# Kernel tuning notes

Measured on AMD Instinct MI355X. Metric: run time of the kernel, lower is better.

The kernel has to match this reference:

```python
import math
import jax, jax.numpy as jnp
import numpy as np

# ---- static config (mirrors init_kwargs) ----
NLAT_I, NLON_I = 240, 480      # input equiangular grid (incl. both poles)
NLAT_O, NLON_O = 361, 720      # output equiangular grid (incl. both poles)
CI, CO = 32, 32
NR, NPHI = 3, 3                # kernel_shape
K = (NR - 1) * NPHI + 1        # anisotropic piecewise-linear DISCO basis size = 7
LMAX = 120
CUTOFF = (NR + 0.25) * math.pi / LMAX     # _compute_cutoff_radius
DLAT_O = math.pi / (NLAT_O - 1)
WOFF = int(math.ceil(CUTOFF / DLAT_O))    # half lat-window (=10); geodesic dist >= |dtheta| so window is exact
WLAT = 2 * WOFF + 1
TWO_PI = 2.0 * math.pi


def _bilinear_upsample(x):
    # ResampleS2(mode='bilinear'): x [B,C,NLAT_I,NLON_I] -> [B,C,NLAT_O,NLON_O]
    # equiangular colatitudes theta_j = pi*j/(nlat-1); periodic longitude.
    pos_t = jnp.linspace(0.0, math.pi, NLAT_O) / (math.pi / (NLAT_I - 1))
    i0 = jnp.clip(jnp.floor(pos_t).astype(jnp.int32), 0, NLAT_I - 1)
    i1 = jnp.minimum(i0 + 1, NLAT_I - 1)
    wt = (pos_t - i0).astype(x.dtype)
    xl = (1.0 - wt)[:, None] * x[:, :, i0, :] + wt[:, None] * x[:, :, i1, :]
    pos_p = (jnp.arange(NLON_O) * (TWO_PI / NLON_O)) / (TWO_PI / NLON_I)
    j0f = jnp.floor(pos_p)
    j0 = j0f.astype(jnp.int32) % NLON_I
    j1 = (j0 + 1) % NLON_I
    wp = (pos_p - j0f).astype(x.dtype)
    return (1.0 - wp) * xl[..., j0] + wp * xl[..., j1]


def _build_psi():
    # DISCO filter tensor psi[k, t_out, dlat, dlon] with quadrature merged in,
    # exploiting longitude translation invariance (computed at lon_out = 0).
    theta = jnp.linspace(0.0, math.pi, NLAT_O)
    t_idx = jnp.arange(NLAT_O)
    d_idx = jnp.arange(WLAT) - WOFF
    lat_in = t_idx[:, None] + d_idx[None, :]             # [T,W]
    valid = (lat_in >= 0) & (lat_in < NLAT_O)
    lat_in_c = jnp.clip(lat_in, 0, NLAT_O - 1)
    alpha = -theta[:, None, None]                         # [T,1,1]
    gamma = theta[lat_in_c][:, :, None]                   # [T,W,1]
    beta = (TWO_PI / NLON_O) * jnp.arange(NLON_O)[None, None, :]
    # rotate input point into frame where the output point is at the north pole
    z = jnp.cos(alpha) * jnp.cos(gamma) - jnp.cos(beta) * jnp.sin(alpha) * jnp.sin(gamma)
    xx = jnp.cos(alpha) * jnp.cos(beta) * jnp.sin(gamma) + jnp.sin(alpha) * jnp.cos(gamma)
    yy = jnp.sin(beta) * jnp.sin(gamma)
    r = jnp.arccos(jnp.clip(z, -1.0, 1.0))                # geodesic distance [T,W,P]
    phi = jnp.arctan2(yy, xx) % TWO_PI                    # local azimuth
    dr = CUTOFF / NR
    dph = TWO_PI / NPHI
    vals = [jnp.maximum(0.0, 1.0 - r / dr)]               # isotropic center hat
    for k in range(1, K):
        ir = (k - 1) // NPHI + 1
        ip = (k - 1) % NPHI
        rad = jnp.maximum(0.0, 1.0 - jnp.abs(r - ir * dr) / dr)
        dd = jnp.abs(phi - ip * dph)
        dd = jnp.minimum(dd, TWO_PI - dd)
        az = jnp.maximum(0.0, 1.0 - dd / dph)
        vals.append(rad * az)
    psi = jnp.stack(vals, 0)                              # [K,T,W,P]
    psi = psi * (r <= CUTOFF) * valid[None, :, :, None]
    # merge quadrature weights of the input grid (sin(theta) dtheta dphi)
    q = jnp.sin(theta) * (math.pi / (NLAT_O - 1)) * (TWO_PI / NLON_O)
    psi = psi * q[lat_in_c][None, :, :, None]
    # nodal L1 normalization per basis function and output node
    scale = jnp.sum(psi, axis=(2, 3), keepdims=True)
    psi = psi / jnp.maximum(scale, 1e-8)
    return psi.astype(jnp.float32), lat_in_c


def _disco_conv(xu, weight, psi, lat_in_c):
    # xu [B,Ci,T,P]; weight [Co,Ci,K]; psi [K,T,W,P]
    h = jnp.einsum('oik,bitp->boktp', weight, xu)         # fold channel mixing first
    Hh = jnp.fft.rfft(h, axis=-1)                         # [B,Co,K,T,F]
    Ph = jnp.conj(jnp.fft.rfft(psi, axis=-1))             # [K,T,W,F]
    yh = jnp.zeros(Hh.shape[:2] + (NLAT_O, Hh.shape[-1]), dtype=Hh.dtype)
    for d in range(WLAT):                                 # small fixed halo loop
        Hd = Hh[:, :, :, lat_in_c[:, d], :]               # [B,Co,K,T,F]
        yh = yh + jnp.einsum('boktf,ktf->botf', Hd, Ph[:, :, d, :])
    return jnp.fft.irfft(yh, n=NLON_O, axis=-1)           # circular correlation over lon


def setup_inputs() -> dict:
    key = jax.random.key(0)
    k1, k2 = jax.random.split(key)
    x = jax.random.normal(k1, (1, CI, NLAT_I, NLON_I), dtype=jnp.float32)
    weight = jax.random.normal(k2, (CO, CI, K), dtype=jnp.float32) * 0.05
    return {'x': x, 'weight': weight}


def reference(x, weight):
    psi, lat_in_c = _build_psi()
    xu = _bilinear_upsample(x.astype(jnp.float32))        # forced fp32 region
    y = _disco_conv(xu, weight.astype(jnp.float32), psi, lat_in_c)
    return y.astype(x.dtype)
```

## Files before the change

kernel.cpp:

```cpp
#include <hip/hip_runtime.h>
#include <hip/hip_bf16.h>
#include <math.h>

#define NLAT_I 240
#define NLON_I 480
#define NLAT_O 361
#define NLON_O 720
#define CI_N 32
#define CO_N 32
#define K_N 7
#define WOFF 10
#define WLAT 21

#define PI_F 3.14159265358979323846f
#define TWOPI_F 6.28318530717958647692f
#define DLAT_V (PI_F / 360.0f)
#define DPHI_V (TWOPI_F / 720.0f)
#define CUTOFF_V (3.25f * PI_F / 120.0f)
#define DR_V (CUTOFF_V / 3.0f)
#define IDR_V (1.0f / DR_V)
#define DPH_V (TWOPI_F / 3.0f)
#define IDPH_V (1.0f / DPH_V)
#define QF_V (DLAT_V * DPHI_V)

#define PAD_T 64
#define CT 64
#define NBLK 512
#define NC45 45
#define NE 7581

typedef __attribute__((ext_vector_type(8))) short short8v;
typedef __attribute__((ext_vector_type(16))) float f32x16;

__device__ __forceinline__ unsigned short f2bf(float f) {
  __hip_bfloat16 h = __float2bfloat16(f);
  union { __hip_bfloat16 b; unsigned short s; } u; u.b = h; return u.s;
}

__device__ __forceinline__ void psi_eval(float ct, float st, float cg, float sg,
                                         float q, float bang, float v[7]) {
  float sb, cb;
  sincosf(bang, &sb, &cb);
  float dx = sg * cb - st;
  float dy = sg * sb;
  float dz = cg - ct;
  float c2 = dx * dx + dy * dy + dz * dz;
  float r = 2.0f * asinf(fminf(1.0f, 0.5f * sqrtf(c2)));
  if (r <= CUTOFF_V) {
    float xx = ct * cb * sg - st * cg;
    float yy = sb * sg;
    float phi = atan2f(yy, xx);
    if (phi < 0.0f) phi += TWOPI_F;
    v[0] = fmaxf(0.0f, 1.0f - r * IDR_V) * q;
#pragma unroll
    for (int k = 1; k < 7; ++k) {
      const float irdr = (float)(1 + (k - 1) / 3) * DR_V;
      const float ipph = (float)((k - 1) % 3) * DPH_V;
      float rad = fmaxf(0.0f, 1.0f - fabsf(r - irdr) * IDR_V);
      float dd = fabsf(phi - ipph);
      dd = fminf(dd, TWOPI_F - dd);
      float az = fmaxf(0.0f, 1.0f - dd * IDPH_V);
      v[k] = rad * az * q;
    }
  } else {
#pragma unroll
    for (int k = 0; k < 7; ++k) v[k] = 0.0f;
  }
}

__device__ __forceinline__ int windowB(int t, int d) {
  int tp = t + d - WOFF;
  if (tp < 0 || tp > NLAT_O - 1) return -1;
  float th = (float)t * DLAT_V, ga = (float)tp * DLAT_V;
  float st = sinf(th), ct = cosf(th), sg = sinf(ga), cg = cosf(ga);
  float den = st * sg;
  float num = cosf(CUTOFF_V) - ct * cg;
  if (den < 1e-9f) return (fabsf(th - ga) <= CUTOFF_V) ? 360 : -1;
  if (num >= den) return -1;
  if (num <= -den) return 360;
  int B = (int)ceilf(acosf(num / den) * (1.0f / DPHI_V)) + 1;
  return B > 360 ? 360 : B;
}

__device__ __forceinline__ int nsupOf(int B) { return (B >= 360) ? 720 : 2 * B + 1; }
__device__ __forceinline__ int widthOf(int B) {
  return (B < 0) ? 0 : ((nsupOf(B) + 129) & ~1);
}

__global__ void prep_kernel(const float* __restrict__ w, unsigned short* __restrict__ w2,
                            int* __restrict__ offsF, int* __restrict__ offsT,
                            int* __restrict__ wtab, float* __restrict__ sums,
                            int* __restrict__ counter) {
  const int tid = threadIdx.x;
  __shared__ int temp[256];
  if (tid == 0) *counter = 0;
  for (int idx = tid; idx < 361 * 7; idx += 256) sums[idx] = 0.0f;
  for (int idx = tid; idx < 14 * 32 * 16; idx += 256) {
    int kk = idx & 15; int o = (idx >> 4) & 31; int c16 = idx >> 9;
    int ci = c16 * 16 + kk; int i = ci & 31; int k = ci >> 5;
    w2[idx] = f2bf(w[(o * 32 + i) * 7 + k]);
  }
  for (int e = tid; e < NE; e += 256) {
    int t = e / 21, d = e % 21;
    int B = windowB(t, d);
    offsF[e] = (B >= 0) ? nsupOf(B) * 7 : 0;
    offsT[e] = 14 * widthOf(B);
  }
  for (int t = tid; t < 361; t += 256) {
    int Wt = 0;
    for (int d = 0; d < WLAT; ++d) {
      int B = windowB(t, d);
      if (B >= 0) Wt += ((31 + B) >> 4) + ((B + 15) >> 4) + 1;
    }
    wtab[t] = Wt;
  }
  __syncthreads();
#pragma unroll 1
  for (int pass = 0; pass < 2; ++pass) {
    int* a = pass ? offsT : offsF;
    int s = tid * 30, e = s + 30; if (e > NE) e = NE; if (s > NE) s = NE;
    int sum = 0;
    for (int i = s; i < e; ++i) sum += a[i];
    temp[tid] = sum;
    __syncthreads();
    if (tid == 0) {
      int run = 0;
      for (int i = 0; i < 256; ++i) { int v = temp[i]; temp[i] = run; run += v; }
      a[NE] = run;
    }
    __syncthreads();
    int run = temp[tid];
    for (int i = s; i < e; ++i) { int v = a[i]; a[i] = run; run += v; }
    __syncthreads();
  }
}

__global__ void upsample_kernel(const float* __restrict__ x,
                                unsigned short* __restrict__ XT) {
  int idx = blockIdx.x * 256 + threadIdx.x;
  if (idx >= NLAT_O * NC45 * 512) return;
  int kk = idx & 15;
  int i = (idx >> 4) & 31;
  int c = (idx >> 9) % NC45;
  int t = idx / (NC45 * 512);
  int p = c * 16 + kk;

  double post = (double)t * (239.0 / 360.0);
  int i0 = (int)floor(post);
  if (i0 < 0) i0 = 0;
  if (i0 > NLAT_I - 1) i0 = NLAT_I - 1;
  int i1 = i0 + 1; if (i1 > NLAT_I - 1) i1 = NLAT_I - 1;
  float wt = (float)(post - (double)i0);

  double posp = (double)p * (2.0 / 3.0);
  double j0f = floor(posp);
  int j0 = ((int)j0f) % NLON_I;
  int j1 = (j0 + 1) % NLON_I;
  float wp = (float)(posp - j0f);

  const float* xi = x + (size_t)i * (NLAT_I * NLON_I);
  float a = xi[i0 * NLON_I + j0];
  float b = xi[i0 * NLON_I + j1];
  float cc = xi[i1 * NLON_I + j0];
  float d = xi[i1 * NLON_I + j1];
  float l0 = (1.0f - wt) * a + wt * cc;
  float l1 = (1.0f - wt) * b + wt * d;
  XT[idx] = f2bf((1.0f - wp) * l0 + wp * l1);
}

__global__ void psi_raw_kernel(const int* __restrict__ offsF,
                               float* __restrict__ PSIF,
                               float* __restrict__ sums) {
  int t = blockIdx.x, d = blockIdx.y;
  int B = windowB(t, d);
  if (B < 0) return;
  int nsup = nsupOf(B);
  int bLo = (B >= 360) ? -360 : -B;
  int offF = offsF[t * 21 + d];
  int tp = t + d - WOFF;
  float th = (float)t * DLAT_V, ga = (float)tp * DLAT_V;
  float st, ct, sg, cg;
  sincosf(th, &st, &ct);
  sincosf(ga, &sg, &cg);
  float q = sg * QF_V;
  float acc[7];
#pragma unroll
  for (int k = 0; k < 7; ++k) acc[k] = 0.0f;
  for (int ix = threadIdx.x; ix < nsup; ix += 256) {
    float v[7];
    psi_eval(ct, st, cg, sg, q, (float)(bLo + ix) * DPHI_V, v);
#pragma unroll
    for (int k = 0; k < 7; ++k) { PSIF[offF + k * nsup + ix] = v[k]; acc[k] += v[k]; }
  }
#pragma unroll
  for (int k = 0; k < 7; ++k) {
    float a = acc[k];
    for (int off = 32; off > 0; off >>= 1) a += __shfl_down(a, off, 64);
    acc[k] = a;
  }
  __shared__ float red[4][7];
  int wid = threadIdx.x >> 6;
  if ((threadIdx.x & 63) == 0) {
#pragma unroll
    for (int k = 0; k < 7; ++k) red[wid][k] = acc[k];
  }
  __syncthreads();
  if (threadIdx.x == 0) {
#pragma unroll
    for (int k = 0; k < 7; ++k)
      atomicAdd(&sums[t * 7 + k], red[0][k] + red[1][k] + red[2][k] + red[3][k]);
  }
}

__global__ void psi_toep_kernel(const int* __restrict__ offsF,
                                const int* __restrict__ offsT,
                                const float* __restrict__ PSIF,
                                const float* __restrict__ sums,
                                unsigned short* __restrict__ PSIT) {
  int t = blockIdx.x, d = blockIdx.y;
  int B = windowB(t, d);
  if (B < 0) return;
  int nsup = nsupOf(B);
  int width = widthOf(B);
  int offF = offsF[t * 21 + d];
  int offT = offsT[t * 21 + d];
  float rc[7];
#pragma unroll
  for (int k = 0; k < 7; ++k) rc[k] = 1.0f / fmaxf(sums[t * 7 + k], 1e-8f);
  for (int ix = threadIdx.x; ix <= width; ix += 256) {
    int isup = ix - PAD_T;
    unsigned short vv[7];
    if (isup >= 0 && isup < nsup) {
#pragma unroll
      for (int k = 0; k < 7; ++k)
        vv[k] = f2bf(PSIF[offF + k * nsup + isup] * rc[k]);
    } else {
#pragma unroll
      for (int k = 0; k < 7; ++k) vv[k] = 0;
    }
    if (ix < width) {
#pragma unroll
      for (int k = 0; k < 7; ++k) PSIT[offT + (2 * k) * width + ix] = vv[k];
    }
    if (ix >= 1) {
#pragma unroll
      for (int k = 0; k < 7; ++k) PSIT[offT + (2 * k + 1) * width + ix - 1] = vv[k];
    }
  }
}

#define LOADSET(S, CC) {                                                  \
    int v45 = pw16 + (CC);                                                \
    if (v45 < 0) v45 += NC45;                                             \
    if (v45 >= NC45) v45 -= NC45;                                         \
    A##S = *(const short8v*)(XT + (((size_t)tpd * NC45 + v45) << 9) + laneA); \
    int jbIdx = (CC) * 16 + lconst - bLo + PAD_T;                         \
    const unsigned short* bp = pbase + jbIdx + ((jbIdx & 1) ? (wdt - 1) : 0); \
    B##S##0 = *(const short8v*)(bp);                                      \
    B##S##1 = *(const short8v*)(bp + ks);                                 \
    B##S##2 = *(const short8v*)(bp + 2 * ks);                             \
    B##S##3 = *(const short8v*)(bp + 3 * ks);                             \
    B##S##4 = *(const short8v*)(bp + 4 * ks);                             \
    B##S##5 = *(const short8v*)(bp + 5 * ks);                             \
    B##S##6 = *(const short8v*)(bp + 6 * ks); }

#define MFMASET(S) {                                                      \
    acc0 = __builtin_amdgcn_mfma_f32_32x32x16_bf16(A##S, B##S##0, acc0, 0, 0, 0); \
    acc1 = __builtin_amdgcn_mfma_f32_32x32x16_bf16(A##S, B##S##1, acc1, 0, 0, 0); \
    acc2 = __builtin_amdgcn_mfma_f32_32x32x16_bf16(A##S, B##S##2, acc2, 0, 0, 0); \
    acc3 = __builtin_amdgcn_mfma_f32_32x32x16_bf16(A##S, B##S##3, acc3, 0, 0, 0); \
    acc4 = __builtin_amdgcn_mfma_f32_32x32x16_bf16(A##S, B##S##4, acc4, 0, 0, 0); \
    acc5 = __builtin_amdgcn_mfma_f32_32x32x16_bf16(A##S, B##S##5, acc5, 0, 0, 0); \
    acc6 = __builtin_amdgcn_mfma_f32_32x32x16_bf16(A##S, B##S##6, acc6, 0, 0, 0); }

#define DUMPQ(RR) {                                                       \
    int iq = ((RR) & 3) + 8 * ((RR) >> 2) + 4 * g;                        \
    int base = nn * 16 + (iq & 15);                                       \
    b2[0*512+base] = f2bf(acc0[RR]); b2[1*512+base] = f2bf(acc1[RR]);     \
    b2[2*512+base] = f2bf(acc2[RR]); b2[3*512+base] = f2bf(acc3[RR]);     \
    b2[4*512+base] = f2bf(acc4[RR]); b2[5*512+base] = f2bf(acc5[RR]);     \
    b2[6*512+base] = f2bf(acc6[RR]); }

__global__ __launch_bounds__(256, 2) void disco_kernel(
    const unsigned short* __restrict__ XT, const unsigned short* __restrict__ PSIT,
    const unsigned short* __restrict__ w2g, const int* __restrict__ offsT,
    const int* __restrict__ wtab, float* __restrict__ y,
    int* __restrict__ counter) {
  const int tid = threadIdx.x;
  __shared__ __align__(16) unsigned short b2all[4 * 3584];
  __shared__ int Sbuf[362];
  __shared__ int sB[WLAT], sUc[WLAT + 1], sOff[WLAT], sW[WLAT];
  __shared__ int curItem;

  for (int j = tid; j < 361; j += 256) {
    int t = (j & 1) ? 360 - (j >> 1) : (j >> 1);
    Sbuf[j] = 6 * ((wtab[t] + CT - 1) / CT);
  }
  __syncthreads();
  if (tid == 0) {
    int run = 0;
    for (int j = 0; j < 361; ++j) { int v = Sbuf[j]; Sbuf[j] = run; run += v; }
    Sbuf[361] = run;
  }
  __syncthreads();
  const int NTOT = Sbuf[361];

  const int lane = tid & 63, wv = tid >> 6, nn = lane & 31, g = lane >> 5;
  const int g8 = g * 8;
  const int laneA = nn * 16 + g8;
  const int lconst = g8 - nn;

  while (true) {
    if (tid == 0) curItem = atomicAdd(counter, 1);
    __syncthreads();
    const int m = curItem;
    if (m >= NTOT) break;

    int lo = 0, hi = 360;
    while (lo < hi) {
      int mid = (lo + hi + 1) >> 1;
      if (Sbuf[mid] <= m) lo = mid; else hi = mid - 1;
    }
    const int j = lo;
    const int r = m - Sbuf[j];
    const int t = (j & 1) ? 360 - (j >> 1) : (j >> 1);
    const int pgroup = r % 6;
    const int part = r / 6;

    if (tid < WLAT) {
      int B = windowB(t, tid);
      sB[tid] = B;
      sOff[tid] = offsT[t * 21 + tid];
      sW[tid] = widthOf(B);
    }
    __syncthreads();
    if (tid == 0) {
      int run = 0; sUc[0] = 0;
      for (int d = 0; d < WLAT; ++d) {
        int B = sB[d];
        int np = (B >= 0) ? ((31 + B) >> 4) + ((B + 15) >> 4) + 1 : 0;
        run += np; sUc[d + 1] = run;
      }
    }
    __syncthreads();
    const int Wt = sUc[WLAT];
    int g0 = part * CT, g1 = g0 + CT;
    if (g1 > Wt) g1 = Wt;

    const int ptile = pgroup * 4 + wv;
    const int pw = ptile * 32;
    const int pw16 = ptile * 2;

    f32x16 acc0, acc1, acc2, acc3, acc4, acc5, acc6;
#pragma unroll
    for (int z = 0; z < 16; ++z) {
      acc0[z]=0; acc1[z]=0; acc2[z]=0; acc3[z]=0; acc4[z]=0; acc5[z]=0; acc6[z]=0;
    }

    short8v A0, A1;
    short8v B00, B01, B02, B03, B04, B05, B06;
    short8v B10, B11, B12, B13, B14, B15, B16;

    int gi = g0;
    int d = 0;
    while (d < WLAT && sUc[d + 1] <= gi) ++d;
    while (gi < g1) {
      const int B = sB[d];
      const int bLo = (B >= 360) ? -360 : -B;
      const int cmin = -((B + 15) >> 4);
      const int tpd = t + d - WOFF;
      const int wdt = sW[d];
      const int ks = 2 * wdt;
      const unsigned short* pbase = PSIT + sOff[d];
      const int rend = sUc[d + 1];
      const int gend = (rend < g1) ? rend : g1;
      const int n = gend - gi;
      int c = cmin + (gi - sUc[d]);

      LOADSET(0, c)
      int it = 0;
      for (; it + 2 <= n; it += 2) {
        LOADSET(1, c + 1)
        MFMASET(0)
        if (it + 2 < n) { LOADSET(0, c + 2) }
        MFMASET(1)
        c += 2;
      }
      if (it < n) { MFMASET(0) }

      gi = gend;
      ++d;
      while (d < WLAT && sUc[d + 1] <= gi) ++d;
    }

    unsigned short* b2 = b2all + wv * 3584;
    f32x16 Dy;
#pragma unroll
    for (int z = 0; z < 16; ++z) Dy[z] = 0.0f;

    {
#pragma unroll
      for (int q2 = 0; q2 < 8; ++q2) { DUMPQ(q2) }
#pragma unroll
      for (int k2 = 0; k2 < 7; ++k2) {
        short8v A2 = *(const short8v*)(w2g + (((2 * k2 + 0) * 32 + nn) << 4) + g8);
        short8v B2f = *(const short8v*)(b2 + (k2 << 9) + (nn << 4) + g8);
        Dy = __builtin_amdgcn_mfma_f32_32x32x16_bf16(A2, B2f, Dy, 0, 0, 0);
      }
    }
    {
#pragma unroll
      for (int q2 = 8; q2 < 16; ++q2) { DUMPQ(q2) }
#pragma unroll
      for (int k2 = 0; k2 < 7; ++k2) {
        short8v A2 = *(const short8v*)(w2g + (((2 * k2 + 1) * 32 + nn) << 4) + g8);
        short8v B2f = *(const short8v*)(b2 + (k2 << 9) + (nn << 4) + g8);
        Dy = __builtin_amdgcn_mfma_f32_32x32x16_bf16(A2, B2f, Dy, 0, 0, 0);
      }
    }

    const int p = pw + nn;
    if (p < NLON_O) {
#pragma unroll
      for (int rr = 0; rr < 16; ++rr) {
        int o = (rr & 3) + 8 * (rr >> 2) + 4 * g;
        atomicAdd(&y[((size_t)o * NLAT_O + t) * NLON_O + p], Dy[rr]);
      }
    }
  }
}

extern "C" void kernel_launch(void* const* d_in, const int* in_sizes, int n_in,
                              void* d_out, int out_size, void* d_ws, size_t ws_size,
                              hipStream_t stream) {
  (void)in_sizes; (void)n_in; (void)out_size; (void)ws_size;
  const float* x = (const float*)d_in[0];
  const float* w = (const float*)d_in[1];
  float* y = (float*)d_out;

  unsigned short* XT = (unsigned short*)d_ws;
  float* PSIF = (float*)(XT + (size_t)NLAT_O * NC45 * 512);
  unsigned short* PSIT = (unsigned short*)(PSIF + 6000000);
  unsigned short* w2 = PSIT + 26000000;
  float* sums = (float*)(w2 + 7168);
  int* offsF = (int*)(sums + NLAT_O * K_N);
  int* offsT = offsF + NE + 1;
  int* wtab = offsT + NE + 1;
  int* counter = wtab + 361;

  hipMemsetAsync(y, 0, (size_t)CO_N * NLAT_O * NLON_O * sizeof(float), stream);

  prep_kernel<<<1, 256, 0, stream>>>(w, w2, offsF, offsT, wtab, sums, counter);
  int n_up = NLAT_O * NC45 * 512;
  upsample_kernel<<<(n_up + 255) / 256, 256, 0, stream>>>(x, XT);
  psi_raw_kernel<<<dim3(NLAT_O, WLAT), 256, 0, stream>>>(offsF, PSIF, sums);
  psi_toep_kernel<<<dim3(NLAT_O, WLAT), 256, 0, stream>>>(offsF, offsT, PSIF, sums, PSIT);
  disco_kernel<<<NBLK, 256, 0, stream>>>(XT, PSIT, w2, offsT, wtab, y, counter);
}
```

Measured before the change: 539.9 us.

## Split basis-K accumulators across two wave groups with 512-thread blocks

The block grows to 8 waves: each longitude tile is handled by two waves, one accumulating basis functions 0-3 and the other 4-6. This cuts accumulator registers per wave from 7 to 4 tiles and deepens the load pipeline to 4 stages. Per-unit Toeplitz offsets are precomputed into shared tables (sMX/sMY), replacing the per-halo-row loop bookkeeping. The two halves of the channel-mix result are exchanged through LDS so each wave issues only half the output atomics. The cost is duplicated A-operand loads, extra block-wide barriers, and more LDS.

```diff
diff --git a/kernel.cpp b/kernel.cpp
--- a/kernel.cpp
+++ b/kernel.cpp
@@ -25,12 +25,15 @@
 
 #define PAD_T 64
 #define CT 64
-#define NBLK 512
+#define NBLK 256
+#define NTHR 512
 #define NC45 45
 #define NE 7581
 
 typedef __attribute__((ext_vector_type(8))) short short8v;
+typedef __attribute__((ext_vector_type(4))) short short4v;
 typedef __attribute__((ext_vector_type(16))) float f32x16;
+typedef __attribute__((ext_vector_type(4))) float f32x4;
 
 __device__ __forceinline__ unsigned short f2bf(float f) {
   __hip_bfloat16 h = __float2bfloat16(f);
@@ -249,52 +252,74 @@
   }
 }
 
-#define LOADSET(S, CC) {                                                  \
-    int v45 = pw16 + (CC);                                                \
-    if (v45 < 0) v45 += NC45;                                             \
-    if (v45 >= NC45) v45 -= NC45;                                         \
-    A##S = *(const short8v*)(XT + (((size_t)tpd * NC45 + v45) << 9) + laneA); \
-    int jbIdx = (CC) * 16 + lconst - bLo + PAD_T;                         \
-    const unsigned short* bp = pbase + jbIdx + ((jbIdx & 1) ? (wdt - 1) : 0); \
-    B##S##0 = *(const short8v*)(bp);                                      \
-    B##S##1 = *(const short8v*)(bp + ks);                                 \
-    B##S##2 = *(const short8v*)(bp + 2 * ks);                             \
-    B##S##3 = *(const short8v*)(bp + 3 * ks);                             \
-    B##S##4 = *(const short8v*)(bp + 4 * ks);                             \
-    B##S##5 = *(const short8v*)(bp + 5 * ks);                             \
-    B##S##6 = *(const short8v*)(bp + 6 * ks); }
-
-#define MFMASET(S) {                                                      \
+
+#define LOADK(S, MI, K4) {                                                    \
+    int mi_ = (MI); if (mi_ >= nU) mi_ = nU - 1;                              \
+    int mx_ = __builtin_amdgcn_readfirstlane(sMX[mi_]);                       \
+    int my_ = __builtin_amdgcn_readfirstlane(sMY[mi_]);                       \
+    int wdt_ = my_ & 4095;                                                    \
+    int dd_ = (my_ >> 12) & 31;                                               \
+    int v45_ = pw16 + ((my_ >> 17) & 63) - 32;                                \
+    if (v45_ < 0) v45_ += NC45; else if (v45_ >= NC45) v45_ -= NC45;          \
+    const unsigned short* ab_ = XT + (((size_t)(t + dd_ - WOFF) * NC45 + v45_) << 9); \
+    A##S = *(const short8v*)(ab_ + laneA);                                    \
+    const unsigned short* bb_ = PSIT + mx_ + kb2 * wdt_;                      \
+    int bo_ = lconst + (((mx_ ^ lconst) & 1) ? (wdt_ - 1) : 0);               \
+    B##S##0 = *(const short8v*)(bb_ + bo_);                                   \
+    B##S##1 = *(const short8v*)(bb_ + 2 * wdt_ + bo_);                        \
+    B##S##2 = *(const short8v*)(bb_ + 4 * wdt_ + bo_);                        \
+    if (K4) { B##S##3 = *(const short8v*)(bb_ + 6 * wdt_ + bo_); } }
+
+#define MFMAK(S, K4) {                                                        \
     acc0 = __builtin_amdgcn_mfma_f32_32x32x16_bf16(A##S, B##S##0, acc0, 0, 0, 0); \
     acc1 = __builtin_amdgcn_mfma_f32_32x32x16_bf16(A##S, B##S##1, acc1, 0, 0, 0); \
     acc2 = __builtin_amdgcn_mfma_f32_32x32x16_bf16(A##S, B##S##2, acc2, 0, 0, 0); \
-    acc3 = __builtin_amdgcn_mfma_f32_32x32x16_bf16(A##S, B##S##3, acc3, 0, 0, 0); \
-    acc4 = __builtin_amdgcn_mfma_f32_32x32x16_bf16(A##S, B##S##4, acc4, 0, 0, 0); \
-    acc5 = __builtin_amdgcn_mfma_f32_32x32x16_bf16(A##S, B##S##5, acc5, 0, 0, 0); \
-    acc6 = __builtin_amdgcn_mfma_f32_32x32x16_bf16(A##S, B##S##6, acc6, 0, 0, 0); }
-
-#define DUMPQ(RR) {                                                       \
-    int iq = ((RR) & 3) + 8 * ((RR) >> 2) + 4 * g;                        \
-    int base = nn * 16 + (iq & 15);                                       \
-    b2[0*512+base] = f2bf(acc0[RR]); b2[1*512+base] = f2bf(acc1[RR]);     \
-    b2[2*512+base] = f2bf(acc2[RR]); b2[3*512+base] = f2bf(acc3[RR]);     \
-    b2[4*512+base] = f2bf(acc4[RR]); b2[5*512+base] = f2bf(acc5[RR]);     \
-    b2[6*512+base] = f2bf(acc6[RR]); }
-
-__global__ __launch_bounds__(256, 2) void disco_kernel(
+    if (K4) { acc3 = __builtin_amdgcn_mfma_f32_32x32x16_bf16(A##S, B##S##3, acc3, 0, 0, 0); } }
+
+#define HOTLOOP(K4)                                                           \
+    LOADK(0, 0, K4) LOADK(1, 1, K4) LOADK(2, 2, K4) LOADK(3, 3, K4)           \
+    {                                                                         \
+      int iu = 0;                                                             \
+      while (iu + 4 <= nU) {                                                  \
+        MFMAK(0, K4) LOADK(0, iu + 4, K4)                                     \
+        MFMAK(1, K4) LOADK(1, iu + 5, K4)                                     \
+        MFMAK(2, K4) LOADK(2, iu + 6, K4)                                     \
+        MFMAK(3, K4) LOADK(3, iu + 7, K4)                                     \
+        iu += 4;                                                              \
+      }                                                                       \
+      if (iu < nU)     { MFMAK(0, K4) }                                       \
+      if (iu + 1 < nU) { MFMAK(1, K4) }                                       \
+      if (iu + 2 < nU) { MFMAK(2, K4) }                                       \
+    }
+
+#define DUMPK(ACC, KABS) {                                                    \
+    int b0_ = ((2 * (KABS)) << 9) + nn * 16 + 4 * g;                          \
+    short4v q_;                                                               \
+    q_[0]=(short)f2bf(ACC[0]);  q_[1]=(short)f2bf(ACC[1]);  q_[2]=(short)f2bf(ACC[2]);  q_[3]=(short)f2bf(ACC[3]);  \
+    *(short4v*)(bp2w + b0_) = q_;                                             \
+    q_[0]=(short)f2bf(ACC[4]);  q_[1]=(short)f2bf(ACC[5]);  q_[2]=(short)f2bf(ACC[6]);  q_[3]=(short)f2bf(ACC[7]);  \
+    *(short4v*)(bp2w + b0_ + 8) = q_;                                         \
+    q_[0]=(short)f2bf(ACC[8]);  q_[1]=(short)f2bf(ACC[9]);  q_[2]=(short)f2bf(ACC[10]); q_[3]=(short)f2bf(ACC[11]); \
+    *(short4v*)(bp2w + b0_ + 512) = q_;                                       \
+    q_[0]=(short)f2bf(ACC[12]); q_[1]=(short)f2bf(ACC[13]); q_[2]=(short)f2bf(ACC[14]); q_[3]=(short)f2bf(ACC[15]); \
+    *(short4v*)(bp2w + b0_ + 512 + 8) = q_; }
+
+__global__ __launch_bounds__(NTHR, 2) void disco_kernel(
     const unsigned short* __restrict__ XT, const unsigned short* __restrict__ PSIT,
     const unsigned short* __restrict__ w2g, const int* __restrict__ offsT,
     const int* __restrict__ wtab, float* __restrict__ y,
     int* __restrict__ counter) {
   const int tid = threadIdx.x;
-  __shared__ __align__(16) unsigned short b2all[4 * 3584];
+  __shared__ __align__(16) unsigned short B2sh[4 * 7168];
+  __shared__ __align__(16) float Xch[4 * 1024];
   __shared__ int Sbuf[362];
   __shared__ int sB[WLAT], sUc[WLAT + 1], sOff[WLAT], sW[WLAT];
+  __shared__ int sMX[CT], sMY[CT];
   __shared__ int curItem;
 
-  for (int j = tid; j < 361; j += 256) {
-    int t = (j & 1) ? 360 - (j >> 1) : (j >> 1);
-    Sbuf[j] = 6 * ((wtab[t] + CT - 1) / CT);
+  for (int j = tid; j < 361; j += NTHR) {
+    int t0 = (j & 1) ? 360 - (j >> 1) : (j >> 1);
+    Sbuf[j] = 6 * ((wtab[t0] + CT - 1) / CT);
   }
   __syncthreads();
   if (tid == 0) {
@@ -309,6 +334,9 @@
   const int g8 = g * 8;
   const int laneA = nn * 16 + g8;
   const int lconst = g8 - nn;
+  const int ptl = wv & 3;
+  const int kg = wv >> 2;
+  const int kb2 = kg * 8;
 
   while (true) {
     if (tid == 0) curItem = atomicAdd(counter, 1);
@@ -346,85 +374,100 @@
     const int Wt = sUc[WLAT];
     int g0 = part * CT, g1 = g0 + CT;
     if (g1 > Wt) g1 = Wt;
-
-    const int ptile = pgroup * 4 + wv;
+    const int nU = g1 - g0;
+
+    if (tid < nU) {
+      int u = g0 + tid;
+      int d = 0;
+      while (sUc[d + 1] <= u) ++d;
+      int B = sB[d];
+      int bLo = (B >= 360) ? -360 : -B;
+      int c = -((B + 15) >> 4) + (u - sUc[d]);
+      sMX[tid] = sOff[d] + c * 16 - bLo + PAD_T;
+      sMY[tid] = sW[d] | (d << 12) | ((c + 32) << 17);
+    }
+    __syncthreads();
+
+    const int ptile = pgroup * 4 + ptl;
     const int pw = ptile * 32;
     const int pw16 = ptile * 2;
 
-    f32x16 acc0, acc1, acc2, acc3, acc4, acc5, acc6;
-#pragma unroll
-    for (int z = 0; z < 16; ++z) {
-      acc0[z]=0; acc1[z]=0; acc2[z]=0; acc3[z]=0; acc4[z]=0; acc5[z]=0; acc6[z]=0;
-    }
-
-    short8v A0, A1;
-    short8v B00, B01, B02, B03, B04, B05, B06;
-    short8v B10, B11, B12, B13, B14, B15, B16;
-
-    int gi = g0;
-    int d = 0;
-    while (d < WLAT && sUc[d + 1] <= gi) ++d;
-    while (gi < g1) {
-      const int B = sB[d];
-      const int bLo = (B >= 360) ? -360 : -B;
-      const int cmin = -((B + 15) >> 4);
-      const int tpd = t + d - WOFF;
-      const int wdt = sW[d];
-      const int ks = 2 * wdt;
-      const unsigned short* pbase = PSIT + sOff[d];
-      const int rend = sUc[d + 1];
-      const int gend = (rend < g1) ? rend : g1;
-      const int n = gend - gi;
-      int c = cmin + (gi - sUc[d]);
-
-      LOADSET(0, c)
-      int it = 0;
-      for (; it + 2 <= n; it += 2) {
-        LOADSET(1, c + 1)
-        MFMASET(0)
-        if (it + 2 < n) { LOADSET(0, c + 2) }
-        MFMASET(1)
-        c += 2;
+    f32x16 acc0, acc1, acc2, acc3;
+#pragma unroll
+    for (int z = 0; z < 16; ++z) { acc0[z] = 0; acc1[z] = 0; acc2[z] = 0; acc3[z] = 0; }
+
+    short8v A0, A1, A2, A3;
+    short8v B00, B01, B02, B03;
+    short8v B10, B11, B12, B13;
+    short8v B20, B21, B22, B23;
+    short8v B30, B31, B32, B33;
+
+    if (kg == 0) { HOTLOOP(1) } else { HOTLOOP(0) }
+
+    unsigned short* bp2w = B2sh + ptl * 7168;
+    if (kg == 0) { DUMPK(acc0, 0) DUMPK(acc1, 1) DUMPK(acc2, 2) DUMPK(acc3, 3) }
+    else         { DUMPK(acc0, 4) DUMPK(acc1, 5) DUMPK(acc2, 6) }
+    __syncthreads();
+
+    f32x16 Dy;
+#pragma unroll
+    for (int z = 0; z < 16; ++z) Dy[z] = 0.0f;
+    {
+      const unsigned short* bp2r = B2sh + ptl * 7168;
+#pragma unroll
+      for (int k2 = 0; k2 < 7; ++k2) {
+        int c16 = 2 * k2 + kg;
+        short8v wa = *(const short8v*)(w2g + ((c16 * 32 + nn) << 4) + g8);
+        short8v gb = *(const short8v*)(bp2r + (c16 << 9) + (nn << 4) + g8);
+        Dy = __builtin_amdgcn_mfma_f32_32x32x16_bf16(wa, gb, Dy, 0, 0, 0);
       }
-      if (it < n) { MFMASET(0) }
-
-      gi = gend;
-      ++d;
-      while (d < WLAT && sUc[d + 1] <= gi) ++d;
-    }
-
-    unsigned short* b2 = b2all + wv * 3584;
-    f32x16 Dy;
-#pragma unroll
-    for (int z = 0; z < 16; ++z) Dy[z] = 0.0f;
-
-    {
-#pragma unroll
-      for (int q2 = 0; q2 < 8; ++q2) { DUMPQ(q2) }
-#pragma unroll
-      for (int k2 = 0; k2 < 7; ++k2) {
-        short8v A2 = *(const short8v*)(w2g + (((2 * k2 + 0) * 32 + nn) << 4) + g8);
-        short8v B2f = *(const short8v*)(b2 + (k2 << 9) + (nn << 4) + g8);
-        Dy = __builtin_amdgcn_mfma_f32_32x32x16_bf16(A2, B2f, Dy, 0, 0, 0);
+    }
+
+    float* xc = Xch + ptl * 1024;
+    if (kg == 0) {
+      f32x4 s0, s1;
+      s0[0] = Dy[8];  s0[1] = Dy[9];  s0[2] = Dy[10]; s0[3] = Dy[11];
+      s1[0] = Dy[12]; s1[1] = Dy[13]; s1[2] = Dy[14]; s1[3] = Dy[15];
+      *(f32x4*)(xc + 512 + lane * 8) = s0;
+      *(f32x4*)(xc + 512 + lane * 8 + 4) = s1;
+    } else {
+      f32x4 s0, s1;
+      s0[0] = Dy[0]; s0[1] = Dy[1]; s0[2] = Dy[2]; s0[3] = Dy[3];
+      s1[0] = Dy[4]; s1[1] = Dy[5]; s1[2] = Dy[6]; s1[3] = Dy[7];
+      *(f32x4*)(xc + lane * 8) = s0;
+      *(f32x4*)(xc + lane * 8 + 4) = s1;
+    }
+    __syncthreads();
+    const int p = pw + nn;
+    if (kg == 0) {
+      f32x4 u0 = *(const f32x4*)(xc + lane * 8);
+      f32x4 u1 = *(const f32x4*)(xc + lane * 8 + 4);
+      if (p < NLON_O) {
+#pragma unroll
+        for (int rr = 0; rr < 4; ++rr) {
+          int o = rr + 4 * g;
+          atomicAdd(&y[((size_t)o * NLAT_O + t) * NLON_O + p], Dy[rr] + u0[rr]);
+        }
+#pragma unroll
+        for (int rr = 4; rr < 8; ++rr) {
+          int o = (rr & 3) + 8 + 4 * g;
+          atomicAdd(&y[((size_t)o * NLAT_O + t) * NLON_O + p], Dy[rr] + u1[rr - 4]);
+        }
       }
-    }
-    {
-#pragma unroll
-      for (int q2 = 8; q2 < 16; ++q2) { DUMPQ(q2) }
-#pragma unroll
-      for (int k2 = 0; k2 < 7; ++k2) {
-        short8v A2 = *(const short8v*)(w2g + (((2 * k2 + 1) * 32 + nn) << 4) + g8);
-        short8v B2f = *(const short8v*)(b2 + (k2 << 9) + (nn << 4) + g8);
-        Dy = __builtin_amdgcn_mfma_f32_32x32x16_bf16(A2, B2f, Dy, 0, 0, 0);
-      }
-    }
-
-    const int p = pw + nn;
-    if (p < NLON_O) {
-#pragma unroll
-      for (int rr = 0; rr < 16; ++rr) {
-        int o = (rr & 3) + 8 * (rr >> 2) + 4 * g;
-        atomicAdd(&y[((size_t)o * NLAT_O + t) * NLON_O + p], Dy[rr]);
+    } else {
+      f32x4 u0 = *(const f32x4*)(xc + 512 + lane * 8);
+      f32x4 u1 = *(const f32x4*)(xc + 512 + lane * 8 + 4);
+      if (p < NLON_O) {
+#pragma unroll
+        for (int rr = 8; rr < 12; ++rr) {
+          int o = (rr & 3) + 16 + 4 * g;
+          atomicAdd(&y[((size_t)o * NLAT_O + t) * NLON_O + p], Dy[rr] + u0[rr - 8]);
+        }
+#pragma unroll
+        for (int rr = 12; rr < 16; ++rr) {
+          int o = (rr & 3) + 24 + 4 * g;
+          atomicAdd(&y[((size_t)o * NLAT_O + t) * NLON_O + p], Dy[rr] + u1[rr - 12]);
+        }
       }
     }
   }
@@ -455,5 +498,5 @@
   upsample_kernel<<<(n_up + 255) / 256, 256, 0, stream>>>(x, XT);
   psi_raw_kernel<<<dim3(NLAT_O, WLAT), 256, 0, stream>>>(offsF, PSIF, sums);
   psi_toep_kernel<<<dim3(NLAT_O, WLAT), 256, 0, stream>>>(offsF, offsT, PSIF, sums, PSIT);
-  disco_kernel<<<NBLK, 256, 0, stream>>>(XT, PSIT, w2, offsT, wtab, y, counter);
-}
+  disco_kernel<<<NBLK, NTHR, 0, stream>>>(XT, PSIT, w2, offsT, wtab, y, counter);
+}
```

Result: slower. 654.2 us (+21.2%).

## Shard work queue per XCD, precompute window tables, vectorize LDS accumulator dump

Applied to the files above, without the earlier changes.

Replaces the single global atomic work counter with eight per-XCD counters. Each block first draws from its own XCD's slice of the item range and then steals from other slices, which cuts contention on one atomic and keeps L2 locality within an XCD. The per-row window bounds and prefix sums are now computed once in the prep kernel and loaded by disco_kernel, instead of being recomputed with trig per item behind an extra barrier. The bf16 accumulator dump to LDS now uses 4-wide short stores in place of scalar stores. The costs are extra workspace tables and a more complex scheduling loop on thread 0.

```diff
diff --git a/kernel.cpp b/kernel.cpp
--- a/kernel.cpp
+++ b/kernel.cpp
@@ -30,6 +30,7 @@
 #define NE 7581
 
 typedef __attribute__((ext_vector_type(8))) short short8v;
+typedef __attribute__((ext_vector_type(4))) short short4v;
 typedef __attribute__((ext_vector_type(16))) float f32x16;
 
 __device__ __forceinline__ unsigned short f2bf(float f) {
@@ -90,10 +91,11 @@
 __global__ void prep_kernel(const float* __restrict__ w, unsigned short* __restrict__ w2,
                             int* __restrict__ offsF, int* __restrict__ offsT,
                             int* __restrict__ wtab, float* __restrict__ sums,
-                            int* __restrict__ counter) {
+                            int* __restrict__ counter, int* __restrict__ gB,
+                            int* __restrict__ gUc) {
   const int tid = threadIdx.x;
   __shared__ int temp[256];
-  if (tid == 0) *counter = 0;
+  if (tid < 8) counter[tid] = 0;
   for (int idx = tid; idx < 361 * 7; idx += 256) sums[idx] = 0.0f;
   for (int idx = tid; idx < 14 * 32 * 16; idx += 256) {
     int kk = idx & 15; int o = (idx >> 4) & 31; int c16 = idx >> 9;
@@ -103,16 +105,21 @@
   for (int e = tid; e < NE; e += 256) {
     int t = e / 21, d = e % 21;
     int B = windowB(t, d);
+    gB[e] = B;
     offsF[e] = (B >= 0) ? nsupOf(B) * 7 : 0;
     offsT[e] = 14 * widthOf(B);
   }
+  __syncthreads();
   for (int t = tid; t < 361; t += 256) {
-    int Wt = 0;
+    int run = 0;
     for (int d = 0; d < WLAT; ++d) {
-      int B = windowB(t, d);
-      if (B >= 0) Wt += ((31 + B) >> 4) + ((B + 15) >> 4) + 1;
-    }
-    wtab[t] = Wt;
+      gUc[t * 22 + d] = run;
+      int B = gB[t * 21 + d];
+      int np = (B >= 0) ? ((31 + B) >> 4) + ((B + 15) >> 4) + 1 : 0;
+      run += np;
+    }
+    gUc[t * 22 + 21] = run;
+    wtab[t] = run;
   }
   __syncthreads();
 #pragma unroll 1
@@ -249,6 +256,7 @@
   }
 }
 
+
 #define LOADSET(S, CC) {                                                  \
     int v45 = pw16 + (CC);                                                \
     if (v45 < 0) v45 += NC45;                                             \
@@ -273,24 +281,26 @@
     acc5 = __builtin_amdgcn_mfma_f32_32x32x16_bf16(A##S, B##S##5, acc5, 0, 0, 0); \
     acc6 = __builtin_amdgcn_mfma_f32_32x32x16_bf16(A##S, B##S##6, acc6, 0, 0, 0); }
 
-#define DUMPQ(RR) {                                                       \
-    int iq = ((RR) & 3) + 8 * ((RR) >> 2) + 4 * g;                        \
-    int base = nn * 16 + (iq & 15);                                       \
-    b2[0*512+base] = f2bf(acc0[RR]); b2[1*512+base] = f2bf(acc1[RR]);     \
-    b2[2*512+base] = f2bf(acc2[RR]); b2[3*512+base] = f2bf(acc3[RR]);     \
-    b2[4*512+base] = f2bf(acc4[RR]); b2[5*512+base] = f2bf(acc5[RR]);     \
-    b2[6*512+base] = f2bf(acc6[RR]); }
+#define DUMP2(ACC, KK, HB) {                                              \
+    short4v q_;                                                           \
+    q_[0]=(short)f2bf(ACC[8*(HB)+0]); q_[1]=(short)f2bf(ACC[8*(HB)+1]);   \
+    q_[2]=(short)f2bf(ACC[8*(HB)+2]); q_[3]=(short)f2bf(ACC[8*(HB)+3]);   \
+    *(short4v*)(b2 + ((KK) << 9) + b0_) = q_;                             \
+    q_[0]=(short)f2bf(ACC[8*(HB)+4]); q_[1]=(short)f2bf(ACC[8*(HB)+5]);   \
+    q_[2]=(short)f2bf(ACC[8*(HB)+6]); q_[3]=(short)f2bf(ACC[8*(HB)+7]);   \
+    *(short4v*)(b2 + ((KK) << 9) + b0_ + 8) = q_; }
 
 __global__ __launch_bounds__(256, 2) void disco_kernel(
     const unsigned short* __restrict__ XT, const unsigned short* __restrict__ PSIT,
     const unsigned short* __restrict__ w2g, const int* __restrict__ offsT,
-    const int* __restrict__ wtab, float* __restrict__ y,
+    const int* __restrict__ wtab, const int* __restrict__ gB,
+    const int* __restrict__ gUc, float* __restrict__ y,
     int* __restrict__ counter) {
   const int tid = threadIdx.x;
   __shared__ __align__(16) unsigned short b2all[4 * 3584];
   __shared__ int Sbuf[362];
   __shared__ int sB[WLAT], sUc[WLAT + 1], sOff[WLAT], sW[WLAT];
-  __shared__ int curItem;
+  __shared__ int curItem, sSv;
 
   for (int j = tid; j < 361; j += 256) {
     int t = (j & 1) ? 360 - (j >> 1) : (j >> 1);
@@ -301,9 +311,11 @@
     int run = 0;
     for (int j = 0; j < 361; ++j) { int v = Sbuf[j]; Sbuf[j] = run; run += v; }
     Sbuf[361] = run;
+    sSv = 0;
   }
   __syncthreads();
   const int NTOT = Sbuf[361];
+  const int xcd = blockIdx.x & 7;
 
   const int lane = tid & 63, wv = tid >> 6, nn = lane & 31, g = lane >> 5;
   const int g8 = g * 8;
@@ -311,7 +323,20 @@
   const int lconst = g8 - nn;
 
   while (true) {
-    if (tid == 0) curItem = atomicAdd(counter, 1);
+    if (tid == 0) {
+      int mm = NTOT;
+      int s2 = sSv;
+      while (s2 < 8) {
+        int cx = (xcd + s2) & 7;
+        int b0 = (NTOT * cx) >> 3;
+        int b1 = (NTOT * (cx + 1)) >> 3;
+        int off = atomicAdd(&counter[cx], 1);
+        if (b0 + off < b1) { mm = b0 + off; break; }
+        ++s2;
+      }
+      sSv = s2;
+      curItem = mm;
+    }
     __syncthreads();
     const int m = curItem;
     if (m >= NTOT) break;
@@ -328,21 +353,14 @@
     const int part = r / 6;
 
     if (tid < WLAT) {
-      int B = windowB(t, tid);
+      int B = gB[t * 21 + tid];
       sB[tid] = B;
       sOff[tid] = offsT[t * 21 + tid];
       sW[tid] = widthOf(B);
     }
+    if (tid < WLAT + 1) sUc[tid] = gUc[t * 22 + tid];
     __syncthreads();
-    if (tid == 0) {
-      int run = 0; sUc[0] = 0;
-      for (int d = 0; d < WLAT; ++d) {
-        int B = sB[d];
-        int np = (B >= 0) ? ((31 + B) >> 4) + ((B + 15) >> 4) + 1 : 0;
-        run += np; sUc[d + 1] = run;
-      }
-    }
-    __syncthreads();
+
     const int Wt = sUc[WLAT];
     int g0 = part * CT, g1 = g0 + CT;
     if (g1 > Wt) g1 = Wt;
@@ -394,13 +412,14 @@
     }
 
     unsigned short* b2 = b2all + wv * 3584;
+    const int b0_ = nn * 16 + 4 * g;
     f32x16 Dy;
 #pragma unroll
     for (int z = 0; z < 16; ++z) Dy[z] = 0.0f;
 
     {
-#pragma unroll
-      for (int q2 = 0; q2 < 8; ++q2) { DUMPQ(q2) }
+      DUMP2(acc0, 0, 0) DUMP2(acc1, 1, 0) DUMP2(acc2, 2, 0) DUMP2(acc3, 3, 0)
+      DUMP2(acc4, 4, 0) DUMP2(acc5, 5, 0) DUMP2(acc6, 6, 0)
 #pragma unroll
       for (int k2 = 0; k2 < 7; ++k2) {
         short8v A2 = *(const short8v*)(w2g + (((2 * k2 + 0) * 32 + nn) << 4) + g8);
@@ -409,8 +428,8 @@
       }
     }
     {
-#pragma unroll
-      for (int q2 = 8; q2 < 16; ++q2) { DUMPQ(q2) }
+      DUMP2(acc0, 0, 1) DUMP2(acc1, 1, 1) DUMP2(acc2, 2, 1) DUMP2(acc3, 3, 1)
+      DUMP2(acc4, 4, 1) DUMP2(acc5, 5, 1) DUMP2(acc6, 6, 1)
 #pragma unroll
       for (int k2 = 0; k2 < 7; ++k2) {
         short8v A2 = *(const short8v*)(w2g + (((2 * k2 + 1) * 32 + nn) << 4) + g8);
@@ -447,13 +466,15 @@
   int* offsT = offsF + NE + 1;
   int* wtab = offsT + NE + 1;
   int* counter = wtab + 361;
+  int* gB = counter + 8;
+  int* gUc = gB + NE;
 
   hipMemsetAsync(y, 0, (size_t)CO_N * NLAT_O * NLON_O * sizeof(float), stream);
 
-  prep_kernel<<<1, 256, 0, stream>>>(w, w2, offsF, offsT, wtab, sums, counter);
+  prep_kernel<<<1, 256, 0, stream>>>(w, w2, offsF, offsT, wtab, sums, counter, gB, gUc);
   int n_up = NLAT_O * NC45 * 512;
   upsample_kernel<<<(n_up + 255) / 256, 256, 0, stream>>>(x, XT);
   psi_raw_kernel<<<dim3(NLAT_O, WLAT), 256, 0, stream>>>(offsF, PSIF, sums);
   psi_toep_kernel<<<dim3(NLAT_O, WLAT), 256, 0, stream>>>(offsF, offsT, PSIF, sums, PSIT);
-  disco_kernel<<<NBLK, 256, 0, stream>>>(XT, PSIT, w2, offsT, wtab, y, counter);
-}
+  disco_kernel<<<NBLK, 256, 0, stream>>>(XT, PSIT, w2, offsT, wtab, gB, gUc, y, counter);
+}
```

New measurement: 522.9 us. 3.1% less time.
